# Optimization experiments

Measured on AMD Instinct MI355X. Metric: run time of the kernel, lower is better.

## Reference

```python
import jax, jax.numpy as jnp
import numpy as np

T, B, IN, H, L = 256, 32, 1024, 1024, 2


def _lstm_layer(x, W, R, bW, bR, y0, c0):
    # x: [T, B, in]; W: [4H, in]; R: [4H, H]; bW/bR: [4H]
    gates_x = jnp.einsum('tbi,gi->tbg', x, W) + (bW + bR)  # [T, B, 4H]

    def step(carry, g):
        y, c = carry
        g = g + y @ R.T                       # [B, 4H]
        i, f, gg, o = jnp.split(g, 4, axis=-1)  # PyTorch gate order i,f,g,o
        i = jax.nn.sigmoid(i)
        f = jax.nn.sigmoid(f)
        gg = jnp.tanh(gg)
        o = jax.nn.sigmoid(o)
        c = f * c + i * gg
        y = o * jnp.tanh(c)
        return (y, c), y

    (yn, cn), ys = jax.lax.scan(step, (y0, c0), gates_x)
    return ys, yn, cn


def setup_inputs() -> dict:
    key = jax.random.key(0)
    ks = jax.random.split(key, 16)
    rsh = 1.0 / np.sqrt(H)
    u = lambda k, shp: jax.random.uniform(k, shp, jnp.float32, -rsh, rsh)
    return {
        'x': jax.random.normal(ks[0], (T, B, IN), jnp.float32),
        'h0': jnp.zeros((L, B, H), jnp.float32),
        'c0': jnp.zeros((L, B, H), jnp.float32),
        'W0': u(ks[1], (4 * H, IN)),
        'R0': u(ks[2], (4 * H, H)),
        'bW0': u(ks[3], (4 * H,)),
        'bR0': u(ks[4], (4 * H,)),
        'W1': u(ks[5], (4 * H, H)),
        'R1': u(ks[6], (4 * H, H)),
        'bW1': u(ks[7], (4 * H,)),
        'bR1': u(ks[8], (4 * H,)),
    }


def reference(x, h0, c0, W0, R0, bW0, bR0, W1, R1, bW1, bR1):
    y1, hn0, cn0 = _lstm_layer(x, W0, R0, bW0, bR0, h0[0], c0[0])
    y2, hn1, cn1 = _lstm_layer(y1, W1, R1, bW1, bR1, h0[1], c0[1])
    h_n = jnp.stack([hn0, hn1])
    c_n = jnp.stack([cn0, cn1])
    return y2, h_n, c_n
```

## Files before the change

kernel.cpp:

```cpp
#include <hip/hip_runtime.h>
#include <hip/hip_bf16.h>

using bf16 = __hip_bfloat16;
typedef __attribute__((ext_vector_type(8))) short short8;
typedef __attribute__((ext_vector_type(4))) float f32x4;

constexpr int kT = 256, kB = 32, kIN = 1024, kH = 1024, kG = 4096;
constexpr int kBH = kB * kH;
constexpr int kNB = kH / 16;

__device__ inline f32x4 mfma16(short8 a, short8 b, f32x4 c) {
    return __builtin_amdgcn_mfma_f32_16x16x32_bf16(a, b, c, 0, 0, 0);
}
__device__ inline short8 ld8(const bf16* p) {
    return *reinterpret_cast<const short8*>(p);
}
__device__ inline float sigmoidf(float x) { return 1.f / (1.f + expf(-x)); }

__global__ void cvt_f32_bf16(const float* __restrict__ in,
                             bf16* __restrict__ outp, int n) {
    for (int i = blockIdx.x * blockDim.x + threadIdx.x; i < n;
         i += gridDim.x * blockDim.x)
        outp[i] = __float2bfloat16(in[i]);
}

__global__ __launch_bounds__(64)
void gemm_bias(const bf16* __restrict__ A, const bf16* __restrict__ Bm,
               const float* __restrict__ b1, const float* __restrict__ b2,
               float* __restrict__ C, int M, int N, int K) {
    const int lane = threadIdx.x;
    const int tn = N >> 6;
    const int bm = blockIdx.x / tn, bn = blockIdx.x - bm * tn;
    const int m0 = bm << 6, n0 = bn << 6;
    const int fr = lane & 15, kq = (lane >> 4) << 3;
    f32x4 acc[4][4];
#pragma unroll
    for (int i = 0; i < 4; i++)
#pragma unroll
        for (int j = 0; j < 4; j++) acc[i][j] = (f32x4){0.f, 0.f, 0.f, 0.f};
    const bf16* Ap = A + (size_t)(m0 + fr) * K + kq;
    const bf16* Bp = Bm + (size_t)(n0 + fr) * K + kq;
    for (int k = 0; k < K; k += 32) {
        short8 af[4], bfr[4];
#pragma unroll
        for (int i = 0; i < 4; i++) af[i] = ld8(Ap + (size_t)(i * 16) * K + k);
#pragma unroll
        for (int i = 0; i < 4; i++) bfr[i] = ld8(Bp + (size_t)(i * 16) * K + k);
#pragma unroll
        for (int i = 0; i < 4; i++)
#pragma unroll
            for (int j = 0; j < 4; j++)
                acc[i][j] = mfma16(af[i], bfr[j], acc[i][j]);
    }
    const int crow = (lane >> 4) << 2, ccol = lane & 15;
#pragma unroll
    for (int j = 0; j < 4; j++) {
        const int nn = n0 + j * 16 + ccol;
        const float bias = b1[nn] + b2[nn];
#pragma unroll
        for (int i = 0; i < 4; i++) {
            const int mm = m0 + i * 16 + crow;
#pragma unroll
            for (int r = 0; r < 4; r++)
                C[(size_t)(mm + r) * N + nn] = acc[i][j][r] + bias;
        }
    }
}

__device__ inline void grid_wait(unsigned* cnt, unsigned tgt) {
    if (threadIdx.x == 0) {
        while (__hip_atomic_load(cnt, __ATOMIC_RELAXED,
                                 __HIP_MEMORY_SCOPE_AGENT) < tgt)
            __builtin_amdgcn_s_sleep(2);
    }
    __syncthreads();
}
__device__ inline void grid_arrive(unsigned* cnt) {
    asm volatile("s_waitcnt vmcnt(0)" ::: "memory");
    __syncthreads();
    if (threadIdx.x == 0)
        __hip_atomic_fetch_add(cnt, 1u, __ATOMIC_RELAXED,
                               __HIP_MEMORY_SCOPE_AGENT);
}
__device__ inline void stage64k(const unsigned* __restrict__ src, char* lds) {
    unsigned v[16];
#pragma unroll
    for (int j = 0; j < 16; j++)
        v[j] = __hip_atomic_load(src + threadIdx.x + 1024 * j,
                                 __ATOMIC_RELAXED, __HIP_MEMORY_SCOPE_AGENT);
#pragma unroll
    for (int j = 0; j < 16; j++) {
        const int byte = (threadIdx.x + 1024 * j) << 2;
        *(unsigned*)(lds + (byte ^ (((byte >> 11) & 7) << 4))) = v[j];
    }
}
__device__ inline void mfma_phase(const char* lds, int a0base, int a1base,
                                  int aswz, const short8* Mf,
                                  f32x4& acc0, f32x4& acc1) {
#pragma unroll
    for (int kk = 0; kk < 8; kk++) {
        const short8 x0 = *(const short8*)(lds + ((a0base + kk * 64) ^ aswz));
        const short8 x1 = *(const short8*)(lds + ((a1base + kk * 64) ^ aswz));
        acc0 = mfma16(x0, Mf[kk], acc0);
        acc1 = mfma16(x1, Mf[kk], acc1);
    }
}

__global__ __launch_bounds__(1024, 1)
void lstm_fused(const float* __restrict__ gx,
                const bf16* __restrict__ R0bf,
                const bf16* __restrict__ W1bf,
                const bf16* __restrict__ R1bf,
                const float* __restrict__ bW1,
                const float* __restrict__ bR1,
                const bf16* __restrict__ h0bf,
                const float* __restrict__ c0,
                bf16* __restrict__ y1seq,
                bf16* __restrict__ y2pp,
                float* __restrict__ outf,
                float* __restrict__ cst,
                unsigned* __restrict__ cntA,
                unsigned* __restrict__ cntB) {
    const int tid = threadIdx.x;
    const bool isA = blockIdx.x < kNB;
    const int bid = blockIdx.x & (kNB - 1);
    const int lane = tid & 63, w = tid >> 6;
    const int g = w & 3, s = w >> 2;
    const int u0 = bid << 4;
    const int fr = lane & 15;
    const int n = g * kH + u0;

    __shared__ __align__(16) char ldsbuf[64 * 1024];
    float* pall = (float*)ldsbuf;

    const int eb = tid >> 3, ecp = (tid & 7) << 1;
    const int crow = (lane >> 4) << 2, ccol = lane & 15;
    const int cbase = s * 512 + (lane >> 4) * 16;
    const int a0base = fr * 2048 + cbase;
    const int a1base = (16 + fr) * 2048 + cbase;
    const int aswz = (fr & 7) << 4;

    if (isA) {
        short8 Rf[8];
        {
            const bf16* Rp = R0bf + (size_t)(n + fr) * kH + s * 256 + (lane >> 4) * 8;
#pragma unroll
            for (int kk = 0; kk < 8; kk++) Rf[kk] = ld8(Rp + kk * 32);
        }
        float creg0 = 0.f, creg1 = 0.f;
        if (tid < 256) {
            creg0 = c0[(size_t)eb * kH + u0 + ecp];
            creg1 = c0[(size_t)eb * kH + u0 + ecp + 1];
        }
#pragma unroll 1
        for (int t = 0; t < kT; t++) {
            if (t) grid_wait(cntA, (unsigned)(kNB * t));
            const unsigned* ysrc = (const unsigned*)(
                t ? y1seq + (size_t)(t - 1) * kBH : h0bf);
            stage64k(ysrc, ldsbuf);
            float e[4][2];
            if (tid < 256) {
                const float* gp = gx + (size_t)t * (kB * kG) + (size_t)eb * kG
                                  + u0 + ecp;
#pragma unroll
                for (int gg = 0; gg < 4; gg++) {
                    e[gg][0] = gp[gg * kH];
                    e[gg][1] = gp[gg * kH + 1];
                }
            }
            __syncthreads();
            f32x4 acc0 = {0.f, 0.f, 0.f, 0.f}, acc1 = {0.f, 0.f, 0.f, 0.f};
            mfma_phase(ldsbuf, a0base, a1base, aswz, Rf, acc0, acc1);
            __syncthreads();
#pragma unroll
            for (int r = 0; r < 4; r++) {
                pall[(((s * 4 + g) * 32) + crow + r) * 17 + ccol] = acc0[r];
                pall[(((s * 4 + g) * 32) + crow + r + 16) * 17 + ccol] = acc1[r];
            }
            __syncthreads();
            if (tid < 256) {
                float v[4][2];
#pragma unroll
                for (int gg = 0; gg < 4; gg++) {
                    float s0 = 0.f, s1 = 0.f;
#pragma unroll
                    for (int ss = 0; ss < 4; ss++) {
                        const int base = ((ss * 4 + gg) * 32 + eb) * 17 + ecp;
                        s0 += pall[base];
                        s1 += pall[base + 1];
                    }
                    v[gg][0] = s0 + e[gg][0];
                    v[gg][1] = s1 + e[gg][1];
                }
                creg0 = sigmoidf(v[1][0]) * creg0 + sigmoidf(v[0][0]) * tanhf(v[2][0]);
                creg1 = sigmoidf(v[1][1]) * creg1 + sigmoidf(v[0][1]) * tanhf(v[2][1]);
                const float y0 = sigmoidf(v[3][0]) * tanhf(creg0);
                const float y1v = sigmoidf(v[3][1]) * tanhf(creg1);
                union { bf16 b[2]; unsigned u; } pk;
                pk.b[0] = __float2bfloat16(y0);
                pk.b[1] = __float2bfloat16(y1v);
                __hip_atomic_store(
                    (unsigned*)(y1seq + (size_t)t * kBH + (size_t)eb * kH + u0 + ecp),
                    pk.u, __ATOMIC_RELAXED, __HIP_MEMORY_SCOPE_AGENT);
            }
            grid_arrive(cntA);
        }
        if (tid < 256) {
            cst[(size_t)eb * kH + u0 + ecp] = creg0;
            cst[(size_t)eb * kH + u0 + ecp + 1] = creg1;
        }
    } else {
        short8 Wf[8], Rf[8];
        {
            const bf16* Wp = W1bf + (size_t)(n + fr) * kH + s * 256 + (lane >> 4) * 8;
            const bf16* Rp = R1bf + (size_t)(n + fr) * kH + s * 256 + (lane >> 4) * 8;
#pragma unroll
            for (int kk = 0; kk < 8; kk++) {
                Wf[kk] = ld8(Wp + kk * 32);
                Rf[kk] = ld8(Rp + kk * 32);
            }
        }
        float creg0 = 0.f, creg1 = 0.f;
        float ebias[4][2];
        if (tid < 256) {
            creg0 = c0[kBH + (size_t)eb * kH + u0 + ecp];
            creg1 = c0[kBH + (size_t)eb * kH + u0 + ecp + 1];
#pragma unroll
            for (int gg = 0; gg < 4; gg++) {
                ebias[gg][0] = bW1[gg * kH + u0 + ecp] + bR1[gg * kH + u0 + ecp];
                ebias[gg][1] = bW1[gg * kH + u0 + ecp + 1] + bR1[gg * kH + u0 + ecp + 1];
            }
        }
#pragma unroll 1
        for (int t = 0; t < kT; t++) {
            grid_wait(cntA, (unsigned)(kNB * (t + 1)));
            stage64k((const unsigned*)(y1seq + (size_t)t * kBH), ldsbuf);
            __syncthreads();
            f32x4 acc0 = {0.f, 0.f, 0.f, 0.f}, acc1 = {0.f, 0.f, 0.f, 0.f};
            mfma_phase(ldsbuf, a0base, a1base, aswz, Wf, acc0, acc1);
            __syncthreads();
            if (t) grid_wait(cntB, (unsigned)(kNB * t));
            const unsigned* y2src = (const unsigned*)(
                t ? y2pp + (size_t)((t - 1) & 1) * kBH : h0bf + kBH);
            stage64k(y2src, ldsbuf);
            __syncthreads();
            mfma_phase(ldsbuf, a0base, a1base, aswz, Rf, acc0, acc1);
            __syncthreads();
#pragma unroll
            for (int r = 0; r < 4; r++) {
                pall[(((s * 4 + g) * 32) + crow + r) * 17 + ccol] = acc0[r];
                pall[(((s * 4 + g) * 32) + crow + r + 16) * 17 + ccol] = acc1[r];
            }
            __syncthreads();
            if (tid < 256) {
                float v[4][2];
#pragma unroll
                for (int gg = 0; gg < 4; gg++) {
                    float s0 = 0.f, s1 = 0.f;
#pragma unroll
                    for (int ss = 0; ss < 4; ss++) {
                        const int base = ((ss * 4 + gg) * 32 + eb) * 17 + ecp;
                        s0 += pall[base];
                        s1 += pall[base + 1];
                    }
                    v[gg][0] = s0 + ebias[gg][0];
                    v[gg][1] = s1 + ebias[gg][1];
                }
                creg0 = sigmoidf(v[1][0]) * creg0 + sigmoidf(v[0][0]) * tanhf(v[2][0]);
                creg1 = sigmoidf(v[1][1]) * creg1 + sigmoidf(v[0][1]) * tanhf(v[2][1]);
                const float y0 = sigmoidf(v[3][0]) * tanhf(creg0);
                const float y1v = sigmoidf(v[3][1]) * tanhf(creg1);
                union { bf16 b[2]; unsigned u; } pk;
                pk.b[0] = __float2bfloat16(y0);
                pk.b[1] = __float2bfloat16(y1v);
                __hip_atomic_store(
                    (unsigned*)(y2pp + (size_t)(t & 1) * kBH + (size_t)eb * kH + u0 + ecp),
                    pk.u, __ATOMIC_RELAXED, __HIP_MEMORY_SCOPE_AGENT);
                float* od = outf + (size_t)t * kBH + (size_t)eb * kH + u0 + ecp;
                od[0] = y0;
                od[1] = y1v;
            }
            if (t != kT - 1) grid_arrive(cntB);
        }
        if (tid < 256) {
            cst[kBH + (size_t)eb * kH + u0 + ecp] = creg0;
            cst[kBH + (size_t)eb * kH + u0 + ecp + 1] = creg1;
        }
    }
}

template <bool FUSED>
__global__ __launch_bounds__(256)
void lstm_step_mfma(const float* __restrict__ gx,
                    const bf16* __restrict__ xbf,
                    const bf16* __restrict__ Wbf,
                    const float* __restrict__ b1,
                    const float* __restrict__ b2,
                    const bf16* __restrict__ Rbf,
                    const bf16* __restrict__ ysrc,
                    bf16* __restrict__ ydst_bf,
                    float* __restrict__ ydst_f,
                    float* __restrict__ cst) {
    const int lane = threadIdx.x & 63, w = threadIdx.x >> 6;
    const int u0 = blockIdx.x << 4;
    const int fr = lane & 15, kq = (lane >> 4) << 3;
    const int n = w * kH + u0;
    f32x4 acc0 = {0.f, 0.f, 0.f, 0.f}, acc1 = {0.f, 0.f, 0.f, 0.f};
    {
        const bf16* Bp = Rbf + (size_t)(n + fr) * kH + kq;
        const bf16* A0 = ysrc + (size_t)fr * kH + kq;
        const bf16* A1 = ysrc + (size_t)(16 + fr) * kH + kq;
#pragma unroll 4
        for (int k = 0; k < kH; k += 32) {
            short8 bfrag = ld8(Bp + k);
            short8 a0 = ld8(A0 + k);
            short8 a1 = ld8(A1 + k);
            acc0 = mfma16(a0, bfrag, acc0);
            acc1 = mfma16(a1, bfrag, acc1);
        }
    }
    if (FUSED) {
        const bf16* Bp = Wbf + (size_t)(n + fr) * kIN + kq;
        const bf16* A0 = xbf + (size_t)fr * kIN + kq;
        const bf16* A1 = xbf + (size_t)(16 + fr) * kIN + kq;
#pragma unroll 4
        for (int k = 0; k < kIN; k += 32) {
            short8 bfrag = ld8(Bp + k);
            short8 a0 = ld8(A0 + k);
            short8 a1 = ld8(A1 + k);
            acc0 = mfma16(a0, bfrag, acc0);
            acc1 = mfma16(a1, bfrag, acc1);
        }
    }
    __shared__ float pre[4][kB][16];
    const int crow = (lane >> 4) << 2, ccol = lane & 15;
#pragma unroll
    for (int r = 0; r < 4; r++) {
        const int b = crow + r;
        float e0, e1;
        if (FUSED) {
            const float bias = b1[n + ccol] + b2[n + ccol];
            e0 = bias; e1 = bias;
        } else {
            e0 = gx[(size_t)b * kG + n + ccol];
            e1 = gx[(size_t)(b + 16) * kG + n + ccol];
        }
        pre[w][b][ccol] = acc0[r] + e0;
        pre[w][b + 16][ccol] = acc1[r] + e1;
    }
    __syncthreads();
    for (int idx = threadIdx.x; idx < kB * 16; idx += 256) {
        const int b = idx >> 4, col = idx & 15;
        const int u = u0 + col;
        const float iv = sigmoidf(pre[0][b][col]);
        const float fv = sigmoidf(pre[1][b][col]);
        const float gv = tanhf(pre[2][b][col]);
        const float ov = sigmoidf(pre[3][b][col]);
        const size_t off = (size_t)b * kH + u;
        const float c = fv * cst[off] + iv * gv;
        const float y = ov * tanhf(c);
        cst[off] = c;
        ydst_bf[off] = __float2bfloat16(y);
        if (ydst_f) ydst_f[off] = y;
    }
}

__global__ void finalize_bf(const bf16* __restrict__ y1last,
                            const float* __restrict__ cst,
                            float* __restrict__ out) {
    const int idx = blockIdx.x * blockDim.x + threadIdx.x;
    if (idx >= 2 * kBH) return;
    const float hv = (idx < kBH)
        ? __bfloat162float(y1last[idx])
        : out[(size_t)(kT - 1) * kBH + (idx - kBH)];
    out[(size_t)kT * kBH + idx] = hv;
    out[(size_t)kT * kBH + 2 * kBH + idx] = cst[idx];
}

__global__ __launch_bounds__(128)
void lstm_step_naive(const float* __restrict__ xA, const float* __restrict__ Wm,
                     const float* __restrict__ bWv, const float* __restrict__ bRv,
                     const float* __restrict__ Rm, const float* __restrict__ ysrc,
                     float* __restrict__ ydst, float* __restrict__ cst) {
    const int tid = threadIdx.x;
    const int b0 = (blockIdx.x & 1) << 4;
    const int bl = tid & 15;
    const int b  = b0 + bl;
    const int u  = ((blockIdx.x >> 1) << 3) + (tid >> 4);
    __shared__ float As[16][129];
    float acc[4] = {0.f, 0.f, 0.f, 0.f};
    const float* wrow[4];
#pragma unroll
    for (int g = 0; g < 4; g++) wrow[g] = Wm + (size_t)(g * kH + u) * 1024;
    for (int k0 = 0; k0 < 1024; k0 += 128) {
        __syncthreads();
        for (int i = tid; i < 16 * 128; i += 128)
            As[i >> 7][i & 127] = xA[(size_t)(b0 + (i >> 7)) * 1024 + k0 + (i & 127)];
        __syncthreads();
#pragma unroll 4
        for (int k = 0; k < 128; k += 4) {
            const float a0 = As[bl][k], a1 = As[bl][k + 1];
            const float a2 = As[bl][k + 2], a3 = As[bl][k + 3];
#pragma unroll
            for (int g = 0; g < 4; g++) {
                const float4 w4 = *reinterpret_cast<const float4*>(wrow[g] + k0 + k);
                acc[g] += a0 * w4.x + a1 * w4.y + a2 * w4.z + a3 * w4.w;
            }
        }
    }
#pragma unroll
    for (int g = 0; g < 4; g++) wrow[g] = Rm + (size_t)(g * kH + u) * 1024;
    for (int k0 = 0; k0 < 1024; k0 += 128) {
        __syncthreads();
        for (int i = tid; i < 16 * 128; i += 128)
            As[i >> 7][i & 127] = ysrc[(size_t)(b0 + (i >> 7)) * 1024 + k0 + (i & 127)];
        __syncthreads();
#pragma unroll 4
        for (int k = 0; k < 128; k += 4) {
            const float a0 = As[bl][k], a1 = As[bl][k + 1];
            const float a2 = As[bl][k + 2], a3 = As[bl][k + 3];
#pragma unroll
            for (int g = 0; g < 4; g++) {
                const float4 w4 = *reinterpret_cast<const float4*>(wrow[g] + k0 + k);
                acc[g] += a0 * w4.x + a1 * w4.y + a2 * w4.z + a3 * w4.w;
            }
        }
    }
#pragma unroll
    for (int g = 0; g < 4; g++) acc[g] += bWv[g * kH + u] + bRv[g * kH + u];
    const float iv = sigmoidf(acc[0]);
    const float fv = sigmoidf(acc[1]);
    const float gv = tanhf(acc[2]);
    const float ov = sigmoidf(acc[3]);
    const size_t off = (size_t)b * kH + u;
    const float c = fv * cst[off] + iv * gv;
    const float y = ov * tanhf(c);
    cst[off] = c;
    ydst[off] = y;
}

__global__ void finalize_f32(const float* __restrict__ y1last,
                             const float* __restrict__ cst,
                             float* __restrict__ out) {
    const int idx = blockIdx.x * blockDim.x + threadIdx.x;
    if (idx >= 2 * kBH) return;
    const float hv = (idx < kBH) ? y1last[idx]
                                 : out[(size_t)(kT - 1) * kBH + (idx - kBH)];
    out[(size_t)kT * kBH + idx] = hv;
    out[(size_t)kT * kBH + 2 * kBH + idx] = cst[idx];
}

extern "C" void kernel_launch(void* const* d_in, const int* in_sizes, int n_in,
                              void* d_out, int out_size, void* d_ws, size_t ws_size,
                              hipStream_t stream) {
    (void)in_sizes; (void)n_in; (void)out_size;
    const float* x   = (const float*)d_in[0];
    const float* h0  = (const float*)d_in[1];
    const float* c0  = (const float*)d_in[2];
    const float* W0  = (const float*)d_in[3];
    const float* R0  = (const float*)d_in[4];
    const float* bW0 = (const float*)d_in[5];
    const float* bR0 = (const float*)d_in[6];
    const float* W1  = (const float*)d_in[7];
    const float* R1  = (const float*)d_in[8];
    const float* bW1 = (const float*)d_in[9];
    const float* bR1 = (const float*)d_in[10];
    float* out = (float*)d_out;
    char* wsp = (char*)d_ws;

    const size_t gxB  = (size_t)kT * kB * kG * 4;
    const size_t xbfB = (size_t)kT * kBH * 2;
    const size_t wB   = (size_t)kG * kH * 2;
    const size_t hbfB = 2 * (size_t)kBH * 2;
    const size_t ppB  = 2 * (size_t)kBH * 2;
    const size_t cstB = 2 * (size_t)kBH * 4;
    const size_t barB = 256;
    const size_t needA = gxB + 2 * xbfB + 4 * wB + hbfB + ppB + cstB + barB;
    const size_t needB = xbfB + 4 * wB + hbfB + 2 * ppB + cstB;

    const dim3 cvB(256), fiG((2 * kBH + 255) / 256);

    if (ws_size >= needA) {
        float* gx    = (float*)wsp;
        bf16*  xbf   = (bf16*)(wsp + gxB);
        bf16*  y1seq = (bf16*)(wsp + gxB + xbfB);
        bf16*  Wb0   = (bf16*)(wsp + gxB + 2 * xbfB);
        bf16*  Rb0   = (bf16*)((char*)Wb0 + wB);
        bf16*  Wb1   = (bf16*)((char*)Wb0 + 2 * wB);
        bf16*  Rb1   = (bf16*)((char*)Wb0 + 3 * wB);
        bf16*  hbf   = (bf16*)((char*)Wb0 + 4 * wB);
        bf16*  y2pp  = (bf16*)((char*)hbf + hbfB);
        float* cst   = (float*)((char*)y2pp + ppB);
        unsigned* bar = (unsigned*)((char*)cst + cstB);

        hipMemsetAsync(bar, 0, barB, stream);
        cvt_f32_bf16<<<dim3(1024), cvB, 0, stream>>>(x, xbf, kT * kBH);
        cvt_f32_bf16<<<dim3(1024), cvB, 0, stream>>>(W0, Wb0, kG * kH);
        cvt_f32_bf16<<<dim3(1024), cvB, 0, stream>>>(R0, Rb0, kG * kH);
        cvt_f32_bf16<<<dim3(1024), cvB, 0, stream>>>(W1, Wb1, kG * kH);
        cvt_f32_bf16<<<dim3(1024), cvB, 0, stream>>>(R1, Rb1, kG * kH);
        cvt_f32_bf16<<<dim3(64), cvB, 0, stream>>>(h0, hbf, 2 * kBH);

        gemm_bias<<<dim3((kT * kB / 64) * (kG / 64)), dim3(64), 0, stream>>>(
            xbf, Wb0, bW0, bR0, gx, kT * kB, kG, kIN);
        lstm_fused<<<dim3(2 * kNB), dim3(1024), 0, stream>>>(
            gx, Rb0, Wb1, Rb1, bW1, bR1, hbf, c0,
            y1seq, y2pp, out, cst, bar, bar + 16);
        finalize_bf<<<fiG, dim3(256), 0, stream>>>(
            y1seq + (size_t)(kT - 1) * kBH, cst, out);
    } else if (ws_size >= needB) {
        bf16*  xbf  = (bf16*)wsp;
        bf16*  Wb0  = (bf16*)(wsp + xbfB);
        bf16*  Rb0  = (bf16*)((char*)Wb0 + wB);
        bf16*  Wb1  = (bf16*)((char*)Wb0 + 2 * wB);
        bf16*  Rb1  = (bf16*)((char*)Wb0 + 3 * wB);
        bf16*  hbf  = (bf16*)((char*)Wb0 + 4 * wB);
        bf16*  y1pp = (bf16*)((char*)hbf + hbfB);
        bf16*  y2pp = (bf16*)((char*)y1pp + ppB);
        float* cst  = (float*)((char*)y2pp + ppB);

        cvt_f32_bf16<<<dim3(1024), cvB, 0, stream>>>(x, xbf, kT * kBH);
        cvt_f32_bf16<<<dim3(1024), cvB, 0, stream>>>(W0, Wb0, kG * kH);
        cvt_f32_bf16<<<dim3(1024), cvB, 0, stream>>>(R0, Rb0, kG * kH);
        cvt_f32_bf16<<<dim3(1024), cvB, 0, stream>>>(W1, Wb1, kG * kH);
        cvt_f32_bf16<<<dim3(1024), cvB, 0, stream>>>(R1, Rb1, kG * kH);
        cvt_f32_bf16<<<dim3(64), cvB, 0, stream>>>(h0, hbf, 2 * kBH);
        hipMemcpyAsync(cst, c0, cstB, hipMemcpyDeviceToDevice, stream);

        for (int t = 0; t < kT; t++) {
            const bf16* ys0 = t ? y1pp + (size_t)((t - 1) & 1) * kBH : hbf;
            bf16* y1t = y1pp + (size_t)(t & 1) * kBH;
            lstm_step_mfma<true><<<dim3(kNB), dim3(256), 0, stream>>>(
                nullptr, xbf + (size_t)t * kBH, Wb0, bW0, bR0,
                Rb0, ys0, y1t, nullptr, cst);
            const bf16* ys1 = t ? y2pp + (size_t)((t - 1) & 1) * kBH : hbf + kBH;
            lstm_step_mfma<true><<<dim3(kNB), dim3(256), 0, stream>>>(
                nullptr, y1t, Wb1, bW1, bR1,
                Rb1, ys1, y2pp + (size_t)(t & 1) * kBH,
                out + (size_t)t * kBH, cst + kBH);
        }
        finalize_bf<<<fiG, dim3(256), 0, stream>>>(
            y1pp + (size_t)((kT - 1) & 1) * kBH, cst, out);
    } else {
        float* y1pp = (float*)wsp;
        float* cst  = y1pp + 2 * (size_t)kBH;
        hipMemcpyAsync(cst, c0, cstB, hipMemcpyDeviceToDevice, stream);
        for (int t = 0; t < kT; t++) {
            const float* ys0 = t ? y1pp + (size_t)((t - 1) & 1) * kBH : h0;
            float* y1t = y1pp + (size_t)(t & 1) * kBH;
            lstm_step_naive<<<dim3(256), dim3(128), 0, stream>>>(
                x + (size_t)t * kB * kIN, W0, bW0, bR0, R0, ys0, y1t, cst);
            const float* ys1 = t ? out + (size_t)(t - 1) * kBH : h0 + kBH;
            lstm_step_naive<<<dim3(256), dim3(128), 0, stream>>>(
                y1t, W1, bW1, bR1, R1, ys1, out + (size_t)t * kBH, cst + kBH);
        }
        finalize_f32<<<fiG, dim3(256), 0, stream>>>(
            y1pp + (size_t)((kT - 1) & 1) * kBH, cst, out);
    }
}
```

Measured before the change: 2.588 ms.

## Split batch across two block groups and merge layer-1 W/R phases

Doubles the persistent grid from 128 to 256 blocks by splitting the batch of 32 rows into two independent 16-row groups, each with its own barrier counters. Each block then stages half as much hidden state and runs a single MFMA tile instead of two. Layer 1 now waits for both its inputs up front, stages y1 and y2 together, and runs the W and R products back to back, dropping one stage/sync round. The trade-off is that each step of layer 1 cannot start its input product before the previous step finishes. The grid also now needs 256 co-resident blocks for the spin barriers to be safe.

```diff
diff --git a/kernel.cpp b/kernel.cpp
--- a/kernel.cpp
+++ b/kernel.cpp
@@ -7,7 +7,7 @@
 
 constexpr int kT = 256, kB = 32, kIN = 1024, kH = 1024, kG = 4096;
 constexpr int kBH = kB * kH;
-constexpr int kNB = kH / 16;
+constexpr int kNB = 64;
 
 __device__ inline f32x4 mfma16(short8 a, short8 b, f32x4 c) {
     return __builtin_amdgcn_mfma_f32_16x16x32_bf16(a, b, c, 0, 0, 0);
@@ -82,28 +82,12 @@
         __hip_atomic_fetch_add(cnt, 1u, __ATOMIC_RELAXED,
                                __HIP_MEMORY_SCOPE_AGENT);
 }
-__device__ inline void stage64k(const unsigned* __restrict__ src, char* lds) {
-    unsigned v[16];
-#pragma unroll
-    for (int j = 0; j < 16; j++)
-        v[j] = __hip_atomic_load(src + threadIdx.x + 1024 * j,
-                                 __ATOMIC_RELAXED, __HIP_MEMORY_SCOPE_AGENT);
-#pragma unroll
-    for (int j = 0; j < 16; j++) {
-        const int byte = (threadIdx.x + 1024 * j) << 2;
-        *(unsigned*)(lds + (byte ^ (((byte >> 11) & 7) << 4))) = v[j];
-    }
-}
-__device__ inline void mfma_phase(const char* lds, int a0base, int a1base,
-                                  int aswz, const short8* Mf,
-                                  f32x4& acc0, f32x4& acc1) {
-#pragma unroll
-    for (int kk = 0; kk < 8; kk++) {
-        const short8 x0 = *(const short8*)(lds + ((a0base + kk * 64) ^ aswz));
-        const short8 x1 = *(const short8*)(lds + ((a1base + kk * 64) ^ aswz));
-        acc0 = mfma16(x0, Mf[kk], acc0);
-        acc1 = mfma16(x1, Mf[kk], acc1);
-    }
+__device__ inline void mfma_phase1(const char* lds, int a0base, int aswz,
+                                   const short8* Mf, f32x4& acc) {
+#pragma unroll
+    for (int kk = 0; kk < 8; kk++)
+        acc = mfma16(*(const short8*)(lds + ((a0base + kk * 64) ^ aswz)),
+                     Mf[kk], acc);
 }
 
 __global__ __launch_bounds__(1024, 1)
@@ -119,26 +103,31 @@
                 bf16* __restrict__ y2pp,
                 float* __restrict__ outf,
                 float* __restrict__ cst,
-                unsigned* __restrict__ cntA,
-                unsigned* __restrict__ cntB) {
+                unsigned* __restrict__ bar) {
     const int tid = threadIdx.x;
-    const bool isA = blockIdx.x < kNB;
-    const int bid = blockIdx.x & (kNB - 1);
+    const bool isA = blockIdx.x < 2 * kNB;
+    const int lid = blockIdx.x & (2 * kNB - 1);
+    const int rg = lid >> 6;
+    const int bid = lid & (kNB - 1);
     const int lane = tid & 63, w = tid >> 6;
     const int g = w & 3, s = w >> 2;
     const int u0 = bid << 4;
+    const int rbase = rg << 4;
     const int fr = lane & 15;
     const int n = g * kH + u0;
 
+    unsigned* cntA = bar + rg * 16;
+    unsigned* cntB = bar + 32 + rg * 16;
+
     __shared__ __align__(16) char ldsbuf[64 * 1024];
     float* pall = (float*)ldsbuf;
 
-    const int eb = tid >> 3, ecp = (tid & 7) << 1;
+    const int er = tid >> 3, ecp = (tid & 7) << 1;
     const int crow = (lane >> 4) << 2, ccol = lane & 15;
     const int cbase = s * 512 + (lane >> 4) * 16;
     const int a0base = fr * 2048 + cbase;
-    const int a1base = (16 + fr) * 2048 + cbase;
     const int aswz = (fr & 7) << 4;
+    const int slice_dw = rbase * 512;
 
     if (isA) {
         short8 Rf[8];
@@ -148,20 +137,29 @@
             for (int kk = 0; kk < 8; kk++) Rf[kk] = ld8(Rp + kk * 32);
         }
         float creg0 = 0.f, creg1 = 0.f;
-        if (tid < 256) {
-            creg0 = c0[(size_t)eb * kH + u0 + ecp];
-            creg1 = c0[(size_t)eb * kH + u0 + ecp + 1];
+        if (tid < 128) {
+            creg0 = c0[(size_t)(rbase + er) * kH + u0 + ecp];
+            creg1 = c0[(size_t)(rbase + er) * kH + u0 + ecp + 1];
         }
 #pragma unroll 1
         for (int t = 0; t < kT; t++) {
             if (t) grid_wait(cntA, (unsigned)(kNB * t));
-            const unsigned* ysrc = (const unsigned*)(
-                t ? y1seq + (size_t)(t - 1) * kBH : h0bf);
-            stage64k(ysrc, ldsbuf);
+            const unsigned* src = (const unsigned*)(
+                t ? y1seq + (size_t)(t - 1) * kBH : h0bf) + slice_dw;
+            unsigned v[8];
+#pragma unroll
+            for (int j = 0; j < 8; j++)
+                v[j] = __hip_atomic_load(src + tid + 1024 * j, __ATOMIC_RELAXED,
+                                         __HIP_MEMORY_SCOPE_AGENT);
+#pragma unroll
+            for (int j = 0; j < 8; j++) {
+                const int byte = (tid + 1024 * j) << 2;
+                *(unsigned*)(ldsbuf + (byte ^ (((byte >> 11) & 7) << 4))) = v[j];
+            }
             float e[4][2];
-            if (tid < 256) {
-                const float* gp = gx + (size_t)t * (kB * kG) + (size_t)eb * kG
-                                  + u0 + ecp;
+            if (tid < 128) {
+                const float* gp = gx + (size_t)t * (kB * kG)
+                                  + (size_t)(rbase + er) * kG + u0 + ecp;
 #pragma unroll
                 for (int gg = 0; gg < 4; gg++) {
                     e[gg][0] = gp[gg * kH];
@@ -169,45 +167,44 @@
                 }
             }
             __syncthreads();
-            f32x4 acc0 = {0.f, 0.f, 0.f, 0.f}, acc1 = {0.f, 0.f, 0.f, 0.f};
-            mfma_phase(ldsbuf, a0base, a1base, aswz, Rf, acc0, acc1);
+            f32x4 acc = {0.f, 0.f, 0.f, 0.f};
+            mfma_phase1(ldsbuf, a0base, aswz, Rf, acc);
             __syncthreads();
 #pragma unroll
-            for (int r = 0; r < 4; r++) {
-                pall[(((s * 4 + g) * 32) + crow + r) * 17 + ccol] = acc0[r];
-                pall[(((s * 4 + g) * 32) + crow + r + 16) * 17 + ccol] = acc1[r];
-            }
+            for (int r = 0; r < 4; r++)
+                pall[(((s * 4 + g) * 16) + crow + r) * 17 + ccol] = acc[r];
             __syncthreads();
-            if (tid < 256) {
-                float v[4][2];
+            if (tid < 128) {
+                float vg[4][2];
 #pragma unroll
                 for (int gg = 0; gg < 4; gg++) {
                     float s0 = 0.f, s1 = 0.f;
 #pragma unroll
                     for (int ss = 0; ss < 4; ss++) {
-                        const int base = ((ss * 4 + gg) * 32 + eb) * 17 + ecp;
+                        const int base = ((ss * 4 + gg) * 16 + er) * 17 + ecp;
                         s0 += pall[base];
                         s1 += pall[base + 1];
                     }
-                    v[gg][0] = s0 + e[gg][0];
-                    v[gg][1] = s1 + e[gg][1];
+                    vg[gg][0] = s0 + e[gg][0];
+                    vg[gg][1] = s1 + e[gg][1];
                 }
-                creg0 = sigmoidf(v[1][0]) * creg0 + sigmoidf(v[0][0]) * tanhf(v[2][0]);
-                creg1 = sigmoidf(v[1][1]) * creg1 + sigmoidf(v[0][1]) * tanhf(v[2][1]);
-                const float y0 = sigmoidf(v[3][0]) * tanhf(creg0);
-                const float y1v = sigmoidf(v[3][1]) * tanhf(creg1);
+                creg0 = sigmoidf(vg[1][0]) * creg0 + sigmoidf(vg[0][0]) * tanhf(vg[2][0]);
+                creg1 = sigmoidf(vg[1][1]) * creg1 + sigmoidf(vg[0][1]) * tanhf(vg[2][1]);
+                const float y0 = sigmoidf(vg[3][0]) * tanhf(creg0);
+                const float y1v = sigmoidf(vg[3][1]) * tanhf(creg1);
                 union { bf16 b[2]; unsigned u; } pk;
                 pk.b[0] = __float2bfloat16(y0);
                 pk.b[1] = __float2bfloat16(y1v);
                 __hip_atomic_store(
-                    (unsigned*)(y1seq + (size_t)t * kBH + (size_t)eb * kH + u0 + ecp),
+                    (unsigned*)(y1seq + (size_t)t * kBH
+                                + (size_t)(rbase + er) * kH + u0 + ecp),
                     pk.u, __ATOMIC_RELAXED, __HIP_MEMORY_SCOPE_AGENT);
             }
             grid_arrive(cntA);
         }
-        if (tid < 256) {
-            cst[(size_t)eb * kH + u0 + ecp] = creg0;
-            cst[(size_t)eb * kH + u0 + ecp + 1] = creg1;
+        if (tid < 128) {
+            cst[(size_t)(rbase + er) * kH + u0 + ecp] = creg0;
+            cst[(size_t)(rbase + er) * kH + u0 + ecp + 1] = creg1;
         }
     } else {
         short8 Wf[8], Rf[8];
@@ -222,9 +219,9 @@
         }
         float creg0 = 0.f, creg1 = 0.f;
         float ebias[4][2];
-        if (tid < 256) {
-            creg0 = c0[kBH + (size_t)eb * kH + u0 + ecp];
-            creg1 = c0[kBH + (size_t)eb * kH + u0 + ecp + 1];
+        if (tid < 128) {
+            creg0 = c0[kBH + (size_t)(rbase + er) * kH + u0 + ecp];
+            creg1 = c0[kBH + (size_t)(rbase + er) * kH + u0 + ecp + 1];
 #pragma unroll
             for (int gg = 0; gg < 4; gg++) {
                 ebias[gg][0] = bW1[gg * kH + u0 + ecp] + bR1[gg * kH + u0 + ecp];
@@ -234,57 +231,74 @@
 #pragma unroll 1
         for (int t = 0; t < kT; t++) {
             grid_wait(cntA, (unsigned)(kNB * (t + 1)));
-            stage64k((const unsigned*)(y1seq + (size_t)t * kBH), ldsbuf);
+            if (t) grid_wait(cntB, (unsigned)(kNB * t));
+            const unsigned* y1src = (const unsigned*)(y1seq + (size_t)t * kBH)
+                                    + slice_dw;
+            const unsigned* y2src = (const unsigned*)(
+                t ? y2pp + (size_t)((t - 1) & 1) * kBH : h0bf + kBH) + slice_dw;
+            unsigned v[16];
+#pragma unroll
+            for (int j = 0; j < 8; j++)
+                v[j] = __hip_atomic_load(y1src + tid + 1024 * j, __ATOMIC_RELAXED,
+                                         __HIP_MEMORY_SCOPE_AGENT);
+#pragma unroll
+            for (int j = 0; j < 8; j++)
+                v[8 + j] = __hip_atomic_load(y2src + tid + 1024 * j, __ATOMIC_RELAXED,
+                                             __HIP_MEMORY_SCOPE_AGENT);
+#pragma unroll
+            for (int j = 0; j < 8; j++) {
+                const int byte = (tid + 1024 * j) << 2;
+                *(unsigned*)(ldsbuf + (byte ^ (((byte >> 11) & 7) << 4))) = v[j];
+            }
+#pragma unroll
+            for (int j = 0; j < 8; j++) {
+                const int byte = 32768 + ((tid + 1024 * j) << 2);
+                *(unsigned*)(ldsbuf + (byte ^ (((byte >> 11) & 7) << 4))) = v[8 + j];
+            }
             __syncthreads();
-            f32x4 acc0 = {0.f, 0.f, 0.f, 0.f}, acc1 = {0.f, 0.f, 0.f, 0.f};
-            mfma_phase(ldsbuf, a0base, a1base, aswz, Wf, acc0, acc1);
+            f32x4 acc = {0.f, 0.f, 0.f, 0.f};
+            mfma_phase1(ldsbuf, a0base, aswz, Wf, acc);
+            mfma_phase1(ldsbuf, 32768 + a0base, aswz, Rf, acc);
             __syncthreads();
-            if (t) grid_wait(cntB, (unsigned)(kNB * t));
-            const unsigned* y2src = (const unsigned*)(
-                t ? y2pp + (size_t)((t - 1) & 1) * kBH : h0bf + kBH);
-            stage64k(y2src, ldsbuf);
+#pragma unroll
+            for (int r = 0; r < 4; r++)
+                pall[(((s * 4 + g) * 16) + crow + r) * 17 + ccol] = acc[r];
             __syncthreads();
-            mfma_phase(ldsbuf, a0base, a1base, aswz, Rf, acc0, acc1);
-            __syncthreads();
-#pragma unroll
-            for (int r = 0; r < 4; r++) {
-                pall[(((s * 4 + g) * 32) + crow + r) * 17 + ccol] = acc0[r];
-                pall[(((s * 4 + g) * 32) + crow + r + 16) * 17 + ccol] = acc1[r];
-            }
-            __syncthreads();
-            if (tid < 256) {
-                float v[4][2];
+            if (tid < 128) {
+                float vg[4][2];
 #pragma unroll
                 for (int gg = 0; gg < 4; gg++) {
                     float s0 = 0.f, s1 = 0.f;
 #pragma unroll
                     for (int ss = 0; ss < 4; ss++) {
-                        const int base = ((ss * 4 + gg) * 32 + eb) * 17 + ecp;
+                        const int base = ((ss * 4 + gg) * 16 + er) * 17 + ecp;
                         s0 += pall[base];
                         s1 += pall[base + 1];
                     }
-                    v[gg][0] = s0 + ebias[gg][0];
-                    v[gg][1] = s1 + ebias[gg][1];
+                    vg[gg][0] = s0 + ebias[gg][0];
+                    vg[gg][1] = s1 + ebias[gg][1];
                 }
-                creg0 = sigmoidf(v[1][0]) * creg0 + sigmoidf(v[0][0]) * tanhf(v[2][0]);
-                creg1 = sigmoidf(v[1][1]) * creg1 + sigmoidf(v[0][1]) * tanhf(v[2][1]);
-                const float y0 = sigmoidf(v[3][0]) * tanhf(creg0);
-                const float y1v = sigmoidf(v[3][1]) * tanhf(creg1);
+                creg0 = sigmoidf(vg[1][0]) * creg0 + sigmoidf(vg[0][0]) * tanhf(vg[2][0]);
+                creg1 = sigmoidf(vg[1][1]) * creg1 + sigmoidf(vg[0][1]) * tanhf(vg[2][1]);
+                const float y0 = sigmoidf(vg[3][0]) * tanhf(creg0);
+                const float y1v = sigmoidf(vg[3][1]) * tanhf(creg1);
                 union { bf16 b[2]; unsigned u; } pk;
                 pk.b[0] = __float2bfloat16(y0);
                 pk.b[1] = __float2bfloat16(y1v);
                 __hip_atomic_store(
-                    (unsigned*)(y2pp + (size_t)(t & 1) * kBH + (size_t)eb * kH + u0 + ecp),
+                    (unsigned*)(y2pp + (size_t)(t & 1) * kBH
+                                + (size_t)(rbase + er) * kH + u0 + ecp),
                     pk.u, __ATOMIC_RELAXED, __HIP_MEMORY_SCOPE_AGENT);
-                float* od = outf + (size_t)t * kBH + (size_t)eb * kH + u0 + ecp;
+                float* od = outf + (size_t)t * kBH + (size_t)(rbase + er) * kH
+                            + u0 + ecp;
                 od[0] = y0;
                 od[1] = y1v;
             }
             if (t != kT - 1) grid_arrive(cntB);
         }
-        if (tid < 256) {
-            cst[kBH + (size_t)eb * kH + u0 + ecp] = creg0;
-            cst[kBH + (size_t)eb * kH + u0 + ecp + 1] = creg1;
+        if (tid < 128) {
+            cst[kBH + (size_t)(rbase + er) * kH + u0 + ecp] = creg0;
+            cst[kBH + (size_t)(rbase + er) * kH + u0 + ecp + 1] = creg1;
         }
     }
 }
@@ -503,9 +517,9 @@
 
         gemm_bias<<<dim3((kT * kB / 64) * (kG / 64)), dim3(64), 0, stream>>>(
             xbf, Wb0, bW0, bR0, gx, kT * kB, kG, kIN);
-        lstm_fused<<<dim3(2 * kNB), dim3(1024), 0, stream>>>(
+        lstm_fused<<<dim3(4 * kNB), dim3(1024), 0, stream>>>(
             gx, Rb0, Wb1, Rb1, bW1, bR1, hbf, c0,
-            y1seq, y2pp, out, cst, bar, bar + 16);
+            y1seq, y2pp, out, cst, bar);
         finalize_bf<<<fiG, dim3(256), 0, stream>>>(
             y1seq + (size_t)(kT - 1) * kBH, cst, out);
     } else if (ws_size >= needB) {
```

Measured after the change: 2.721 ms. 5.1% more time.
